# Performance work log

Hardware: AMD Instinct MI355X
Metric: run time of the kernel (lower is better)

## Reference

```python
import jax, jax.numpy as jnp
import numpy as np

NMS_KS = 15
TOP_K = 2048
GAUSS_KS = 7
GAUSS_SIGMA = 1.0
LOSS_LAMBDA = 1.0


def setup_inputs() -> dict:
    key = jax.random.key(0)
    k1, k2, k3 = jax.random.split(key, 3)
    B, H, W = 16, 1024, 1024
    score1 = jax.random.uniform(k1, (B, 1, H, W), dtype=jnp.float32)
    w_score2 = jax.random.uniform(k2, (B, 1, H, W), dtype=jnp.float32)
    w_vis_mask2 = jax.random.randint(k3, (B, 1, H, W), 0, 2) > 0
    return {"score1": score1, "w_score2": w_score2, "w_vis_mask2": w_vis_mask2}


def _nms(score, ks):
    # keep only local maxima within a ks x ks window (stride 1, 'same' padding)
    pooled = jax.lax.reduce_window(score, -jnp.inf, jax.lax.max,
                                   (1, 1, ks, ks), (1, 1, 1, 1), 'SAME')
    return jnp.where(score == pooled, score, jnp.zeros_like(score))


def _prepare_gt_score(score, nms_ks, k, mask):
    # NMS -> mask -> per-image top-k -> binary GT keypoint map
    s = _nms(score, nms_ks) * mask.astype(score.dtype)
    b = s.shape[0]
    flat = s.reshape(b, -1)                      # B x (H*W)
    _, idx = jax.lax.top_k(flat, k)              # B x k
    gt = jnp.zeros_like(flat).at[jnp.arange(b)[:, None], idx].set(1.0)
    return gt.reshape(s.shape)


def _gaussian_filter(x, ks, sigma):
    coords = jnp.arange(ks, dtype=jnp.float32) - (ks - 1) / 2.0
    g = jnp.exp(-(coords ** 2) / (2.0 * sigma ** 2))
    g = g / g.sum()
    k2d = jnp.outer(g, g)[None, None]
    pad = ks // 2
    return jax.lax.conv_general_dilated(
        x, k2d, (1, 1), [(pad, pad), (pad, pad)],
        dimension_numbers=('NCHW', 'OIHW', 'NCHW'))


def reference(score1, w_score2, w_vis_mask2):
    b = score1.shape[0]
    gt_score1 = jax.lax.stop_gradient(
        _prepare_gt_score(w_score2, NMS_KS, TOP_K, w_vis_mask2))
    gt_score1 = _gaussian_filter(gt_score1, GAUSS_KS, GAUSS_SIGMA)
    m = w_vis_mask2.astype(jnp.float32)
    loss = ((score1 - gt_score1) ** 2) * m       # masked elementwise MSE
    loss = loss.reshape(b, -1).sum(-1) / jnp.clip(m.reshape(b, -1).sum(-1), 1e-8)
    return LOSS_LAMBDA * loss.mean()
```

## Files before the change

kernel.cpp:

```cpp
#include <hip/hip_runtime.h>
#include <math.h>

#define BATCH 16
#define H 1024
#define W 1024
#define HR 46
#define CGW 20
#define CGP 21
#define NTILES 8192
#define CAP 4096
#define TOPK 2048
#define BCAP 40

struct WS {
  double term1[BATCH];
  double corr[BATCH];
  unsigned int masksum[BATCH];
  int cand_count[BATCH];
  int   tile_cnt[NTILES];
  float pt1[NTILES * 4];
  int   pmc[NTILES * 4];
  float tile_val[NTILES * BCAP];
  int   tile_idx[NTILES * BCAP];
  float ccand_val[BATCH * CAP];
  int   ccand_idx[BATCH * CAP];
};

__constant__ float GW[7] = {
  0.004433048175f, 0.054005582623f, 0.242036229376f, 0.399050279652f,
  0.242036229376f, 0.054005582623f, 0.004433048175f
};

__device__ __forceinline__ float4 max4(float4 a, float4 b) {
  float4 r;
  r.x = fmaxf(a.x, b.x); r.y = fmaxf(a.y, b.y);
  r.z = fmaxf(a.z, b.z); r.w = fmaxf(a.w, b.w);
  return r;
}

__global__ void k_zero(WS* ws) {
  const int g = blockIdx.x * 256 + threadIdx.x;
  ((float4*)ws->ccand_val)[g] = make_float4(0.f, 0.f, 0.f, 0.f);
  if (g < 2048) ((int4*)ws->tile_cnt)[g] = make_int4(0, 0, 0, 0);
  if (blockIdx.x == 0 && threadIdx.x < BATCH) {
    const int t = threadIdx.x;
    ws->term1[t] = 0.0;
    ws->corr[t] = 0.0;
    ws->masksum[t] = 0u;
    ws->cand_count[t] = 0;
  }
}

__global__ __launch_bounds__(256, 6) void k_nms(const float* __restrict__ score1,
                                                const float* __restrict__ score2,
                                                const int* __restrict__ mask,
                                                WS* __restrict__ ws) {
  __shared__ float4 halo[HR][CGP];
  __shared__ float4 rmax[32][CGP];
  const int tid = threadIdx.x;

  const int t = blockIdx.x;
  const int b  = t >> 9;
  const int tt = t & 511;
  const int ty0 = (tt >> 4) << 5;
  const int tx0 = (tt & 15) << 6;
  const size_t ibase = (size_t)b * ((size_t)H * W);

  float4 st[4];
  int hr_[4], hc_[4];
  const bool interior = (ty0 >= 7) && (ty0 + 38 < H) && (tx0 >= 8) && (tx0 + 71 < W);
  if (interior) {
    #pragma unroll
    for (int k = 0; k < 4; k++) {
      int i = tid + (k << 8);
      if (i < HR * CGW) {
        int r = i / CGW, c = i - r * CGW;
        hr_[k] = r; hc_[k] = c;
        st[k] = *((const float4*)(score2 + ibase + (size_t)(ty0 - 7 + r) * W + (tx0 - 8)) + c);
      }
    }
  } else {
    #pragma unroll
    for (int k = 0; k < 4; k++) {
      int i = tid + (k << 8);
      if (i < HR * CGW) {
        int r = i / CGW, c = i - r * CGW;
        hr_[k] = r; hc_[k] = c;
        int gy = ty0 - 7 + r, gx = tx0 - 8 + (c << 2);
        float vv[4] = {-INFINITY, -INFINITY, -INFINITY, -INFINITY};
        if (gy >= 0 && gy < H) {
          const float* rp = score2 + ibase + (size_t)gy * W;
          #pragma unroll
          for (int u = 0; u < 4; u++) {
            int gxu = gx + u;
            if (gxu >= 0 && gxu < W) vv[u] = rp[gxu];
          }
        }
        st[k] = make_float4(vv[0], vv[1], vv[2], vv[3]);
      }
    }
  }
  const int prow = tid >> 3;
  const int c8   = tid & 7;
  const size_t pb = ibase + (size_t)(ty0 + prow) * W + tx0 + (c8 << 3);
  const float4 s1a = *(const float4*)(score1 + pb);
  const float4 s1b = *(const float4*)(score1 + pb + 4);
  const int4  mka = *(const int4*)(mask + pb);
  const int4  mkb = *(const int4*)(mask + pb + 4);

  #pragma unroll
  for (int k = 0; k < 4; k++) {
    int i = tid + (k << 8);
    if (i < HR * CGW) halo[hr_[k]][hc_[k]] = st[k];
  }
  __syncthreads();

  if (tid < 160) {
    const int rr = tid / 20;
    const int cg = tid - rr * 20;
    const int R0 = rr << 2;
    float4 core = halo[R0 + 3][cg];
    #pragma unroll
    for (int k = 4; k <= 14; k++) core = max4(core, halo[R0 + k][cg]);
    const float4 h0 = halo[R0][cg], h1 = halo[R0 + 1][cg], h2 = halo[R0 + 2][cg];
    const float4 h15 = halo[R0 + 15][cg], h16 = halo[R0 + 16][cg], h17 = halo[R0 + 17][cg];
    const float4 p2 = h2, p1 = max4(h1, p2), p0 = max4(h0, p1);
    const float4 sf15 = h15, sf16 = max4(sf15, h16), sf17 = max4(sf16, h17);
    rmax[R0 + 0][cg] = max4(core, p0);
    rmax[R0 + 1][cg] = max4(max4(core, p1), sf15);
    rmax[R0 + 2][cg] = max4(max4(core, p2), sf16);
    rmax[R0 + 3][cg] = max4(core, sf17);
  }

  float t1 = 0.f; int mcnt = 0; unsigned int mbits = 0;
  {
    const float sc[8] = {s1a.x, s1a.y, s1a.z, s1a.w, s1b.x, s1b.y, s1b.z, s1b.w};
    const int   mm[8] = {mka.x, mka.y, mka.z, mka.w, mkb.x, mkb.y, mkb.z, mkb.w};
    #pragma unroll
    for (int j = 0; j < 8; j++) {
      if (mm[j]) { t1 = fmaf(sc[j], sc[j], t1); mcnt++; mbits |= (1u << j); }
    }
  }
  __syncthreads();

  float r[24];
  #pragma unroll
  for (int g = 0; g < 6; g++) {
    float4 v = rmax[prow][(c8 << 1) + g];
    r[4 * g + 0] = v.x; r[4 * g + 1] = v.y; r[4 * g + 2] = v.z; r[4 * g + 3] = v.w;
  }
  float core = r[8];
  #pragma unroll
  for (int k = 9; k <= 15; k++) core = fmaxf(core, r[k]);
  const float q7 = r[7];
  const float q6 = fmaxf(r[6], q7);
  const float q5 = fmaxf(r[5], q6);
  const float q4 = fmaxf(r[4], q5);
  const float q3 = fmaxf(r[3], q4);
  const float q2 = fmaxf(r[2], q3);
  const float q1 = fmaxf(r[1], q2);
  float sa[7];
  sa[0] = r[16];
  #pragma unroll
  for (int k = 1; k < 7; k++) sa[k] = fmaxf(sa[k - 1], r[16 + k]);
  float pooled[8];
  pooled[0] = fmaxf(core, q1);
  pooled[1] = fmaxf(fmaxf(core, q2), sa[0]);
  pooled[2] = fmaxf(fmaxf(core, q3), sa[1]);
  pooled[3] = fmaxf(fmaxf(core, q4), sa[2]);
  pooled[4] = fmaxf(fmaxf(core, q5), sa[3]);
  pooled[5] = fmaxf(fmaxf(core, q6), sa[4]);
  pooled[6] = fmaxf(fmaxf(core, q7), sa[5]);
  pooled[7] = fmaxf(core, sa[6]);

  const float4 cva = halo[prow + 7][(c8 << 1) + 2];
  const float4 cvb = halo[prow + 7][(c8 << 1) + 3];
  const float cc[8] = {cva.x, cva.y, cva.z, cva.w, cvb.x, cvb.y, cvb.z, cvb.w};
  #pragma unroll
  for (int j = 0; j < 8; j++) {
    if ((mbits >> j) & 1u) {
      const float s = cc[j];
      if (s == pooled[j] && s > 0.f) {
        int slot = atomicAdd(&ws->tile_cnt[t], 1);
        if (slot < BCAP) {
          ws->tile_val[t * BCAP + slot] = s;
          ws->tile_idx[t * BCAP + slot] = (ty0 + prow) * W + tx0 + (c8 << 3) + j;
        }
      }
    }
  }
  #pragma unroll
  for (int off = 32; off > 0; off >>= 1) {
    t1 += __shfl_down(t1, off);
    mcnt += __shfl_down(mcnt, off);
  }
  if ((tid & 63) == 0) {
    ws->pt1[t * 4 + (tid >> 6)] = t1;
    ws->pmc[t * 4 + (tid >> 6)] = mcnt;
  }
}

__global__ __launch_bounds__(256) void k_compact(WS* __restrict__ ws) {
  const int b = blockIdx.x;
  const int tid = threadIdx.x;
  const int lane = tid & 63, w = tid >> 6;
  __shared__ double sF[4];
  __shared__ int    sI[4];
  __shared__ int    wt[4];

  double tsum = 0.0; int msum = 0;
  for (int j = tid; j < 2048; j += 256) {
    tsum += (double)ws->pt1[b * 2048 + j];
    msum += ws->pmc[b * 2048 + j];
  }
  #pragma unroll
  for (int off = 32; off > 0; off >>= 1) {
    tsum += __shfl_down(tsum, off);
    msum += __shfl_down(msum, off);
  }
  if (lane == 0) { sF[w] = tsum; sI[w] = msum; }

  const int tg = b * 512 + 2 * tid;
  int c0 = ws->tile_cnt[tg];     if (c0 > BCAP) c0 = BCAP;
  int c1 = ws->tile_cnt[tg + 1]; if (c1 > BCAP) c1 = BCAP;
  const int pairs = c0 + c1;
  int v = pairs;
  #pragma unroll
  for (int off = 1; off < 64; off <<= 1) {
    int u = __shfl_up(v, off);
    if (lane >= off) v += u;
  }
  if (lane == 63) wt[w] = v;
  __syncthreads();
  if (tid == 0) {
    ws->term1[b] = (sF[0] + sF[1]) + (sF[2] + sF[3]);
    ws->masksum[b] = (unsigned int)(sI[0] + sI[1] + sI[2] + sI[3]);
  }
  int wo = 0;
  #pragma unroll
  for (int k = 0; k < 4; k++) if (k < w) wo += wt[k];
  const int excl = v - pairs + wo;
  if (tid == 255) {
    int tot = excl + pairs;
    ws->cand_count[b] = (tot > CAP) ? CAP : tot;
  }
  float* dv = ws->ccand_val + b * CAP;
  int*   di = ws->ccand_idx + b * CAP;
  const float* sv0 = ws->tile_val + (size_t)tg * BCAP;
  const int*   si0 = ws->tile_idx + (size_t)tg * BCAP;
  for (int j = 0; j < c0; j++) {
    int o = excl + j;
    if (o < CAP) { dv[o] = sv0[j]; di[o] = si0[j]; }
  }
  for (int j = 0; j < c1; j++) {
    int o = excl + c0 + j;
    if (o < CAP) { dv[o] = sv0[BCAP + j]; di[o] = si0[BCAP + j]; }
  }
}

__global__ __launch_bounds__(256, 4) void k_rankstamp(const float* __restrict__ score1,
                                                      const int* __restrict__ mask,
                                                      WS* __restrict__ ws) {
  const int b = blockIdx.x >> 6;
  const int slice = blockIdx.x & 63;
  int n = ws->cand_count[b]; if (n > CAP) n = CAP;
  const int i0 = slice << 6;
  if (i0 >= n) return;
  __shared__ __align__(16) float sval[CAP];
  __shared__ __align__(16) int   sidx[CAP];
  __shared__ int   s_prank[4][64];
  __shared__ int   s_keys[64];
  __shared__ int   s_nk;
  __shared__ float cred[4];
  const int tid = threadIdx.x;
  const int nf4 = (n + 3) >> 2;

  const float4* gv = (const float4*)(ws->ccand_val + b * CAP);
  const int4*   gi = (const int4*)(ws->ccand_idx + b * CAP);
  for (int j = tid; j < nf4; j += 256) {
    ((float4*)sval)[j] = gv[j];
    ((int4*)sidx)[j]   = gi[j];
  }
  __syncthreads();

  const int w = tid >> 6, l = tid & 63;
  const float vi = sval[i0 + l];
  const int   xi = sidx[i0 + l];
  const int q = (nf4 + 3) >> 2;
  int lo = w * q; if (lo > nf4) lo = nf4;
  int hi = lo + q; if (hi > nf4) hi = nf4;
  int rank = 0;
  int j = lo;
  for (; j + 4 <= hi; j += 4) {
    #pragma unroll
    for (int u = 0; u < 4; u++) {
      const float4 v = ((const float4*)sval)[j + u];
      const int4  iv = ((const int4*)sidx)[j + u];
      rank += (v.x > vi) + (v.y > vi) + (v.z > vi) + (v.w > vi);
      rank += (v.x == vi && iv.x < xi);
      rank += (v.y == vi && iv.y < xi);
      rank += (v.z == vi && iv.z < xi);
      rank += (v.w == vi && iv.w < xi);
    }
  }
  for (; j < hi; j++) {
    const float4 v = ((const float4*)sval)[j];
    const int4  iv = ((const int4*)sidx)[j];
    rank += (v.x > vi) + (v.y > vi) + (v.z > vi) + (v.w > vi);
    rank += (v.x == vi && iv.x < xi);
    rank += (v.y == vi && iv.y < xi);
    rank += (v.z == vi && iv.z < xi);
    rank += (v.w == vi && iv.w < xi);
  }
  s_prank[w][l] = rank;
  __syncthreads();

  if (tid < 64) {
    const int rtot = s_prank[0][tid] + s_prank[1][tid] + s_prank[2][tid] + s_prank[3][tid];
    const bool sel = (i0 + tid < n) && (rtot < TOPK);
    const unsigned long long bal = __ballot(sel);
    if (sel) {
      const int pos = __popcll(bal & ((1ull << tid) - 1ull));
      s_keys[pos] = sidx[i0 + tid];
    }
    if (tid == 0) s_nk = (int)__popcll(bal);
  }
  __syncthreads();
  const int nk = s_nk;

  float contrib = 0.f;
  const int sub = tid & 7;
  const size_t ib2 = (size_t)b * ((size_t)H * W);
  #pragma unroll
  for (int rnd = 0; rnd < 2; rnd++) {
    const int k = (tid >> 3) + (rnd << 5);
    if (k < nk && sub < 7) {
      const int ck = s_keys[k];
      const int cy = ck >> 10, cx = ck & 1023;
      const int py = cy + sub - 3;
      const float wy = GW[sub] * ((py >= 0 && py < H) ? 1.f : 0.f);
      const int pyc = min(max(py, 0), H - 1);
      const float* s1r = score1 + ib2 + (size_t)pyc * W;
      const int*   mr  = mask   + ib2 + (size_t)pyc * W;
      #pragma unroll
      for (int dx = -3; dx <= 3; dx++) {
        const int px = cx + dx;
        const float wv = wy * GW[dx + 3] * ((px >= 0 && px < W) ? 1.f : 0.f);
        const int pxc = min(max(px, 0), W - 1);
        const float mf = (mr[pxc] != 0) ? 1.f : 0.f;
        contrib += mf * wv * (wv - 2.f * s1r[pxc]);
      }
    }
  }
  #pragma unroll
  for (int off = 32; off > 0; off >>= 1) contrib += __shfl_down(contrib, off);
  if ((tid & 63) == 0) cred[tid >> 6] = contrib;
  __syncthreads();
  if (tid == 0)
    atomicAdd(&ws->corr[b], (double)((cred[0] + cred[1]) + (cred[2] + cred[3])));
}

__global__ void k_final(WS* __restrict__ ws, float* __restrict__ out) {
  const int t = threadIdx.x;
  double v = 0.0;
  if (t < BATCH) {
    double denom = (double)ws->masksum[t];
    if (denom < 1e-8) denom = 1e-8;
    v = (ws->term1[t] + ws->corr[t]) / denom;
  }
  #pragma unroll
  for (int off = 32; off > 0; off >>= 1) v += __shfl_down(v, off);
  if (t == 0) out[0] = (float)(v / BATCH);
}

extern "C" void kernel_launch(void* const* d_in, const int* in_sizes, int n_in,
                              void* d_out, int out_size, void* d_ws, size_t ws_size,
                              hipStream_t stream) {
  const float* score1 = (const float*)d_in[0];
  const float* score2 = (const float*)d_in[1];
  const int*   mask   = (const int*)d_in[2];
  float* out = (float*)d_out;
  WS* ws = (WS*)d_ws;

  k_zero<<<64, 256, 0, stream>>>(ws);
  k_nms<<<NTILES, 256, 0, stream>>>(score1, score2, mask, ws);
  k_compact<<<BATCH, 256, 0, stream>>>(ws);
  k_rankstamp<<<BATCH * 64, 256, 0, stream>>>(score1, mask, ws);
  k_final<<<1, 64, 0, stream>>>(ws, out);
}
```

Baseline: 101.0 us.

## Stage NMS candidates in LDS, drop zeroing kernel, remap blocks across XCDs

Each NMS tile now collects its candidates in shared memory with a shared-memory atomic counter and writes the count and the list to global memory once, so global atomics on tile counters are no longer needed. That removes the separate zeroing kernel: k_compact now resets corr and zero-pads the three slots past the candidate tail itself. Block indices in k_nms and k_rankstamp are permuted so consecutive tiles land on the same XCD, aiming for better L2 locality. The change saves one launch and the global atomic traffic, at the cost of an extra __syncthreads per NMS block.

```diff
diff --git a/kernel.cpp b/kernel.cpp
--- a/kernel.cpp
+++ b/kernel.cpp
@@ -38,33 +38,25 @@
   return r;
 }
 
-__global__ void k_zero(WS* ws) {
-  const int g = blockIdx.x * 256 + threadIdx.x;
-  ((float4*)ws->ccand_val)[g] = make_float4(0.f, 0.f, 0.f, 0.f);
-  if (g < 2048) ((int4*)ws->tile_cnt)[g] = make_int4(0, 0, 0, 0);
-  if (blockIdx.x == 0 && threadIdx.x < BATCH) {
-    const int t = threadIdx.x;
-    ws->term1[t] = 0.0;
-    ws->corr[t] = 0.0;
-    ws->masksum[t] = 0u;
-    ws->cand_count[t] = 0;
-  }
-}
-
 __global__ __launch_bounds__(256, 6) void k_nms(const float* __restrict__ score1,
                                                 const float* __restrict__ score2,
                                                 const int* __restrict__ mask,
                                                 WS* __restrict__ ws) {
   __shared__ float4 halo[HR][CGP];
   __shared__ float4 rmax[32][CGP];
+  __shared__ float s_cv[BCAP];
+  __shared__ int   s_ci[BCAP];
+  __shared__ int   s_cnt;
   const int tid = threadIdx.x;
 
-  const int t = blockIdx.x;
+  const int t = (blockIdx.x & 7) * (NTILES / 8) + (blockIdx.x >> 3);
   const int b  = t >> 9;
   const int tt = t & 511;
   const int ty0 = (tt >> 4) << 5;
   const int tx0 = (tt & 15) << 6;
   const size_t ibase = (size_t)b * ((size_t)H * W);
+
+  if (tid == 0) s_cnt = 0;
 
   float4 st[4];
   int hr_[4], hc_[4];
@@ -181,10 +173,10 @@
     if ((mbits >> j) & 1u) {
       const float s = cc[j];
       if (s == pooled[j] && s > 0.f) {
-        int slot = atomicAdd(&ws->tile_cnt[t], 1);
+        int slot = atomicAdd(&s_cnt, 1);
         if (slot < BCAP) {
-          ws->tile_val[t * BCAP + slot] = s;
-          ws->tile_idx[t * BCAP + slot] = (ty0 + prow) * W + tx0 + (c8 << 3) + j;
+          s_cv[slot] = s;
+          s_ci[slot] = (ty0 + prow) * W + tx0 + (c8 << 3) + j;
         }
       }
     }
@@ -197,6 +189,13 @@
   if ((tid & 63) == 0) {
     ws->pt1[t * 4 + (tid >> 6)] = t1;
     ws->pmc[t * 4 + (tid >> 6)] = mcnt;
+  }
+  __syncthreads();
+  int cnt = s_cnt; if (cnt > BCAP) cnt = BCAP;
+  if (tid == 0) ws->tile_cnt[t] = cnt;
+  if (tid < cnt) {
+    ws->tile_val[t * BCAP + tid] = s_cv[tid];
+    ws->tile_idx[t * BCAP + tid] = s_ci[tid];
   }
 }
 
@@ -235,17 +234,22 @@
   if (tid == 0) {
     ws->term1[b] = (sF[0] + sF[1]) + (sF[2] + sF[3]);
     ws->masksum[b] = (unsigned int)(sI[0] + sI[1] + sI[2] + sI[3]);
+    ws->corr[b] = 0.0;
   }
   int wo = 0;
   #pragma unroll
   for (int k = 0; k < 4; k++) if (k < w) wo += wt[k];
   const int excl = v - pairs + wo;
+  float* dv = ws->ccand_val + b * CAP;
+  int*   di = ws->ccand_idx + b * CAP;
   if (tid == 255) {
     int tot = excl + pairs;
-    ws->cand_count[b] = (tot > CAP) ? CAP : tot;
-  }
-  float* dv = ws->ccand_val + b * CAP;
-  int*   di = ws->ccand_idx + b * CAP;
+    if (tot > CAP) tot = CAP;
+    ws->cand_count[b] = tot;
+    #pragma unroll
+    for (int u = 0; u < 3; u++)
+      if (tot + u < CAP) dv[tot + u] = 0.f;
+  }
   const float* sv0 = ws->tile_val + (size_t)tg * BCAP;
   const int*   si0 = ws->tile_idx + (size_t)tg * BCAP;
   for (int j = 0; j < c0; j++) {
@@ -261,8 +265,9 @@
 __global__ __launch_bounds__(256, 4) void k_rankstamp(const float* __restrict__ score1,
                                                       const int* __restrict__ mask,
                                                       WS* __restrict__ ws) {
-  const int b = blockIdx.x >> 6;
-  const int slice = blockIdx.x & 63;
+  const int blk = (blockIdx.x & 7) * 128 + (blockIdx.x >> 3);
+  const int b = blk >> 6;
+  const int slice = blk & 63;
   int n = ws->cand_count[b]; if (n > CAP) n = CAP;
   const int i0 = slice << 6;
   if (i0 >= n) return;
@@ -382,7 +387,6 @@
   float* out = (float*)d_out;
   WS* ws = (WS*)d_ws;
 
-  k_zero<<<64, 256, 0, stream>>>(ws);
   k_nms<<<NTILES, 256, 0, stream>>>(score1, score2, mask, ws);
   k_compact<<<BATCH, 256, 0, stream>>>(ws);
   k_rankstamp<<<BATCH * 64, 256, 0, stream>>>(score1, mask, ws);
```

Measured after the change: 82.26 us (median of 2 runs). 18.6% less time.
